# Kernel tuning notes

Hardware: AMD Instinct MI355X
Metric: run time of the kernel (lower is better)

## Reference

```python
import jax, jax.numpy as jnp
import numpy as np

DIM = 192
NUM_HEADS = 6
WINDOW = (2, 6, 12)
INPUT_RES = (8, 48, 180)
TYPE_OF_WINDOWS = (INPUT_RES[0] // WINDOW[0]) * (INPUT_RES[1] // WINDOW[1])  # 32
N_TOK = WINDOW[0] * WINDOW[1] * WINDOW[2]  # 144
NLON = INPUT_RES[2] // WINDOW[2]  # 15
TABLE_ROWS = WINDOW[0] ** 2 * WINDOW[1] ** 2 * (2 * WINDOW[2] - 1)  # 3312


def calculate_position_bias_indices(ws):
    wz, wh, ww = ws
    zi = np.arange(wz)
    zj = -np.arange(wz) * wz
    hi = np.arange(wh)
    hj = -np.arange(wh) * wh
    w = np.arange(ww)
    c1 = np.stack(np.meshgrid(zi, hi, w, indexing='ij')).reshape(3, -1)
    c2 = np.stack(np.meshgrid(zj, hj, w, indexing='ij')).reshape(3, -1)
    coords = (c1[:, :, None] - c2[:, None, :]).transpose(1, 2, 0).copy()
    coords[:, :, 2] += ww - 1
    coords[:, :, 1] *= 2 * ww - 1
    coords[:, :, 0] *= (2 * ww - 1) * wh * wh
    return coords.sum(-1)  # (N, N) in [0, TABLE_ROWS)


def setup_inputs() -> dict:
    key = jax.random.key(0)
    ks = jax.random.split(key, 7)
    B_ = NLON  # batch=1 times nLon window columns
    x = jax.random.normal(ks[0], (B_, TYPE_OF_WINDOWS, N_TOK, DIM), dtype=jnp.float32)
    mask = jax.random.normal(ks[1], (NLON, TYPE_OF_WINDOWS, N_TOK, N_TOK), dtype=jnp.float32)
    qkv_w = jax.random.normal(ks[2], (3 * DIM, DIM), dtype=jnp.float32) * 0.02
    qkv_b = jax.random.normal(ks[3], (3 * DIM,), dtype=jnp.float32) * 0.02
    proj_w = jax.random.normal(ks[4], (DIM, DIM), dtype=jnp.float32) * 0.02
    proj_b = jax.random.normal(ks[5], (DIM,), dtype=jnp.float32) * 0.02
    bias_table = jax.random.normal(ks[6], (TABLE_ROWS, TYPE_OF_WINDOWS, NUM_HEADS), dtype=jnp.float32) * 0.02
    position_index = jnp.asarray(calculate_position_bias_indices(WINDOW), dtype=jnp.int64)
    return {"x": x, "mask": mask, "qkv_w": qkv_w, "qkv_b": qkv_b,
            "proj_w": proj_w, "proj_b": proj_b, "bias_table": bias_table,
            "position_index": position_index}


def reference(x, mask, qkv_w, qkv_b, proj_w, proj_b, bias_table, position_index):
    B_, nW_, N, C = x.shape
    H = NUM_HEADS
    hd = C // H
    scale = hd ** (-0.5)
    # qkv projection: (B_, nW_, N, 3, H, hd)
    qkv = (jnp.einsum('bwnc,dc->bwnd', x, qkv_w) + qkv_b).reshape(B_, nW_, N, 3, H, hd)
    q = qkv[:, :, :, 0] * scale  # (B_, nW_, N, H, hd)
    k = qkv[:, :, :, 1]
    v = qkv[:, :, :, 2]
    # attention scores: (B_, H, nW_, N, N)
    attn = jnp.einsum('bwihd,bwjhd->bhwij', q, k)
    # gathered earth position bias -> (H, nW_, N, N)
    bias = bias_table[position_index.reshape(-1)]  # (N*N, nW_, H)
    bias = bias.reshape(N, N, nW_, H).transpose(3, 2, 0, 1)
    attn = attn + bias[None]
    # mask add: view (B_//nLon, nLon, H, nW_, N, N) + mask (nLon, 1, nW_, N, N)
    nLon = mask.shape[0]
    attn = attn.reshape(B_ // nLon, nLon, H, nW_, N, N) + mask[None, :, None]
    attn = attn.reshape(B_, H, nW_, N, N)
    attn = jax.nn.softmax(attn, axis=-1)
    out = jnp.einsum('bhwij,bwjhd->bwihd', attn, v).reshape(B_, nW_, N, C)
    out = jnp.einsum('bwnc,dc->bwnd', out, proj_w) + proj_b
    return out
```

## Files before the change

### kernel.cpp

```cpp
#include <hip/hip_runtime.h>
#include <hip/hip_bf16.h>

#define B_LON 15
#define NW    32
#define NTOK  144
#define DIM   192
#define NH    6
#define HD    32
#define K3    576
#define MROWS (B_LON*NW*NTOK)
#define NN    (NTOK*NTOK)
#define SCALE 0.17677669529663687f

typedef __attribute__((ext_vector_type(8))) short bf16x8;
typedef __attribute__((ext_vector_type(8))) unsigned short u16x8;
typedef __attribute__((ext_vector_type(4))) float f32x4;

__device__ inline unsigned short f2bf(float f) {
  __bf16 h = (__bf16)f;
  return __builtin_bit_cast(unsigned short, h);
}
__device__ inline float bf2f(unsigned short u) {
  union { unsigned int i; float f; } c;
  c.i = ((unsigned int)u) << 16;
  return c.f;
}

#define NX8 1658880
#define NQ8 13824
#define NP8 4608

__global__ __launch_bounds__(256) void conv_bf_k(
    const float* __restrict__ x, const float* __restrict__ qw,
    const float* __restrict__ pw,
    unsigned short* __restrict__ xbf, unsigned short* __restrict__ qwbf,
    unsigned short* __restrict__ pwbf) {
  const long gid = (long)blockIdx.x * 256 + threadIdx.x;
  const float* src;
  unsigned short* dst;
  long off;
  if (gid < NX8)            { src = x;  dst = xbf;  off = gid; }
  else if (gid < NX8 + NQ8) { src = qw; dst = qwbf; off = gid - NX8; }
  else                      { src = pw; dst = pwbf; off = gid - NX8 - NQ8; }
  const float4 a = ((const float4*)src)[off * 2];
  const float4 b = ((const float4*)src)[off * 2 + 1];
  u16x8 u = {f2bf(a.x), f2bf(a.y), f2bf(a.z), f2bf(a.w),
             f2bf(b.x), f2bf(b.y), f2bf(b.z), f2bf(b.w)};
  *(u16x8*)&dst[off * 8] = u;
}

__global__ __launch_bounds__(256) void bias_pre_k(
    const float* __restrict__ btab, const int* __restrict__ pos,
    unsigned short* __restrict__ biasb) {
  const int wh  = blockIdx.x;
  const int seg = blockIdx.y * 2304;
  unsigned short* dst = biasb + (size_t)wh * NN;
#pragma unroll
  for (int it = 0; it < 9; ++it) {
    const int e = seg + it * 256 + threadIdx.x;
    dst[e] = f2bf(btab[(size_t)pos[e] * (NW * NH) + wh]);
  }
}

__global__ __launch_bounds__(256) void qkv_gemm_k(
    const unsigned short* __restrict__ X, const unsigned short* __restrict__ W,
    const float* __restrict__ Bv,
    unsigned short* __restrict__ qb, unsigned short* __restrict__ kb,
    unsigned short* __restrict__ vb) {
  __shared__ unsigned short As[256 * 72];
  __shared__ unsigned short Bs[64 * 72];
  const int t    = threadIdx.x;
  const int n0   = blockIdx.x * 64;
  const int m0   = blockIdx.y * 256;
  const int w    = t >> 6;
  const int lane = t & 63;
  const int ln15 = lane & 15;
  const int quad = lane >> 4;
  const int srow = t >> 3;
  const int schk = (t & 7) * 8;

  f32x4 acc[4][4];
#pragma unroll
  for (int i = 0; i < 4; ++i)
#pragma unroll
    for (int j = 0; j < 4; ++j) acc[i][j] = (f32x4){0.f, 0.f, 0.f, 0.f};

  for (int k0 = 0; k0 < 192; k0 += 64) {
    u16x8 ar[8], br[2];
#pragma unroll
    for (int rr = 0; rr < 8; ++rr)
      ar[rr] = *(const u16x8*)&X[(size_t)(m0 + rr * 32 + srow) * 192 + k0 + schk];
#pragma unroll
    for (int rr = 0; rr < 2; ++rr)
      br[rr] = *(const u16x8*)&W[(size_t)(n0 + rr * 32 + srow) * 192 + k0 + schk];
    __syncthreads();
#pragma unroll
    for (int rr = 0; rr < 8; ++rr)
      *(u16x8*)&As[(rr * 32 + srow) * 72 + schk] = ar[rr];
#pragma unroll
    for (int rr = 0; rr < 2; ++rr)
      *(u16x8*)&Bs[(rr * 32 + srow) * 72 + schk] = br[rr];
    __syncthreads();

#pragma unroll
    for (int half = 0; half < 2; ++half) {
      bf16x8 af[4], bf[4];
#pragma unroll
      for (int mt = 0; mt < 4; ++mt)
        af[mt] = *(bf16x8*)&As[(w * 64 + mt * 16 + ln15) * 72 + half * 32 + quad * 8];
#pragma unroll
      for (int nt = 0; nt < 4; ++nt)
        bf[nt] = *(bf16x8*)&Bs[(nt * 16 + ln15) * 72 + half * 32 + quad * 8];
#pragma unroll
      for (int mt = 0; mt < 4; ++mt)
#pragma unroll
        for (int nt = 0; nt < 4; ++nt)
          acc[mt][nt] = __builtin_amdgcn_mfma_f32_16x16x32_bf16(
              af[mt], bf[nt], acc[mt][nt], 0, 0, 0);
    }
    __syncthreads();
  }

  const int s   = n0 / 192;
  const int nr  = n0 % 192;
  const float sc2 = (s == 0) ? SCALE : 1.0f;
  unsigned short* dst = (s == 0) ? qb : (s == 1 ? kb : vb);
#pragma unroll
  for (int nt = 0; nt < 4; ++nt) {
    const int colg = n0 + nt * 16 + ln15;
    const int h    = (nr + nt * 16 + ln15) >> 5;
    const int dd   = (nr + nt * 16 + ln15) & 31;
    const float bias = Bv[colg];
#pragma unroll
    for (int mt = 0; mt < 4; ++mt) {
#pragma unroll
      for (int r = 0; r < 4; ++r) {
        const int m  = m0 + w * 64 + mt * 16 + quad * 4 + r;
        const int bw = m / NTOK;
        const int n  = m % NTOK;
        const unsigned short val = f2bf((acc[mt][nt][r] + bias) * sc2);
        if (s < 2)
          dst[((size_t)(bw * NH + h) * NTOK + n) * HD + dd] = val;
        else
          dst[((size_t)(bw * NH + h) * HD + dd) * NTOK + n] = val;
      }
    }
  }
}

__global__ __launch_bounds__(192, 3) void attn_k(
    const unsigned short* __restrict__ qbuf, const unsigned short* __restrict__ kbuf,
    const unsigned short* __restrict__ vbuf, const float* __restrict__ mask,
    const unsigned short* __restrict__ biasb, unsigned short* __restrict__ ao) {
  __shared__ unsigned short Ks[NTOK * 36];
  __shared__ unsigned short Vs[32 * 160];
  __shared__ unsigned short Ps[3 * 16 * 168];

  const int t    = threadIdx.x;
  const int wave = t / 64;
  const int lane = t & 63;
  const int ln15 = lane & 15;
  const int quad = lane >> 4;
  const int idx  = blockIdx.x;
  const int h    = idx / 480;
  const int bw   = idx % 480;
  const int w    = bw & 31;
  const int wh   = w * NH + h;
  const size_t hb = (size_t)(bw * NH + h) * (NTOK * HD);
  const unsigned short* qh = qbuf + hb;
  const float* maskp = mask + (size_t)bw * NN;
  const unsigned short* biasp = biasb + (size_t)wh * NN;
  unsigned short* ps = &Ps[wave * 16 * 168];

  for (int it = t; it < 576; it += 192) {
    const int row = it >> 2;
    const int col = (it & 3) * 8;
    *(u16x8*)&Ks[row * 36 + col] = *(const u16x8*)&kbuf[hb + row * HD + col];
  }
  for (int it = t; it < 576; it += 192) {
    const int row = it / 18;
    const int col = (it % 18) * 8;
    *(u16x8*)&Vs[row * 160 + col] = *(const u16x8*)&vbuf[hb + row * NTOK + col];
  }
  if (t < 64) {
    u16x8 z = {0, 0, 0, 0, 0, 0, 0, 0};
    *(u16x8*)&Vs[(t >> 1) * 160 + 144 + (t & 1) * 8] = z;
  }
  {
    ushort4 z = {0, 0, 0, 0};
    *(ushort4*)&ps[(lane >> 2) * 168 + 144 + (lane & 3) * 4] = z;
  }
  __syncthreads();

  for (int g = wave * 3; g < wave * 3 + 3; ++g) {
    const int i0 = g * 16;
    const int ib = i0 + quad * 4;

    const bf16x8 qf = *(const bf16x8*)&qh[(i0 + ln15) * HD + quad * 8];
    f32x4 s[9];
#pragma unroll
    for (int jt = 0; jt < 9; ++jt) {
      const bf16x8 kf = *(const bf16x8*)&Ks[(jt * 16 + ln15) * 36 + quad * 8];
      s[jt] = (f32x4){0.f, 0.f, 0.f, 0.f};
      s[jt] = __builtin_amdgcn_mfma_f32_16x16x32_bf16(qf, kf, s[jt], 0, 0, 0);
    }

#pragma unroll
    for (int jt = 0; jt < 9; ++jt) {
      const int j = jt * 16 + ln15;
#pragma unroll
      for (int r = 0; r < 4; ++r) {
        const int ij = (ib + r) * NTOK + j;
        s[jt][r] += bf2f(biasp[ij]) + maskp[ij];
      }
    }

    float rinv[4];
#pragma unroll
    for (int r = 0; r < 4; ++r) {
      float mx = s[0][r];
#pragma unroll
      for (int jt = 1; jt < 9; ++jt) mx = fmaxf(mx, s[jt][r]);
#pragma unroll
      for (int off = 1; off < 16; off <<= 1) mx = fmaxf(mx, __shfl_xor(mx, off));
      float sum = 0.f;
#pragma unroll
      for (int jt = 0; jt < 9; ++jt) {
        const float e = __expf(s[jt][r] - mx);
        s[jt][r] = e;
        sum += e;
      }
#pragma unroll
      for (int off = 1; off < 16; off <<= 1) sum += __shfl_xor(sum, off);
      rinv[r] = 1.0f / sum;
    }

#pragma unroll
    for (int jt = 0; jt < 9; ++jt)
#pragma unroll
      for (int r = 0; r < 4; ++r)
        ps[(quad * 4 + r) * 168 + jt * 16 + ln15] = f2bf(s[jt][r]);

    f32x4 o[2] = {{0.f, 0.f, 0.f, 0.f}, {0.f, 0.f, 0.f, 0.f}};
#pragma unroll
    for (int kt = 0; kt < 5; ++kt) {
      const bf16x8 pf = *(const bf16x8*)&ps[ln15 * 168 + kt * 32 + quad * 8];
#pragma unroll
      for (int nt = 0; nt < 2; ++nt) {
        const bf16x8 vf = *(const bf16x8*)&Vs[(nt * 16 + ln15) * 160 + kt * 32 + quad * 8];
        o[nt] = __builtin_amdgcn_mfma_f32_16x16x32_bf16(pf, vf, o[nt], 0, 0, 0);
      }
    }

#pragma unroll
    for (int nt = 0; nt < 2; ++nt)
#pragma unroll
      for (int r = 0; r < 4; ++r)
        ao[(size_t)(bw * NTOK + ib + r) * DIM + h * HD + nt * 16 + ln15] =
            f2bf(o[nt][r] * rinv[r]);
  }
}

__global__ __launch_bounds__(256) void proj_gemm_k(
    const unsigned short* __restrict__ AO, const unsigned short* __restrict__ W,
    const float* __restrict__ Bv, float* __restrict__ out) {
  __shared__ unsigned short As[256 * 72];
  __shared__ unsigned short Bs[64 * 72];
  const int t    = threadIdx.x;
  const int n0   = blockIdx.x * 64;
  const int m0   = blockIdx.y * 256;
  const int w    = t >> 6;
  const int lane = t & 63;
  const int ln15 = lane & 15;
  const int quad = lane >> 4;
  const int srow = t >> 3;
  const int schk = (t & 7) * 8;

  f32x4 acc[4][4];
#pragma unroll
  for (int i = 0; i < 4; ++i)
#pragma unroll
    for (int j = 0; j < 4; ++j) acc[i][j] = (f32x4){0.f, 0.f, 0.f, 0.f};

  for (int k0 = 0; k0 < 192; k0 += 64) {
    u16x8 ar[8], br[2];
#pragma unroll
    for (int rr = 0; rr < 8; ++rr)
      ar[rr] = *(const u16x8*)&AO[(size_t)(m0 + rr * 32 + srow) * 192 + k0 + schk];
#pragma unroll
    for (int rr = 0; rr < 2; ++rr)
      br[rr] = *(const u16x8*)&W[(size_t)(n0 + rr * 32 + srow) * 192 + k0 + schk];
    __syncthreads();
#pragma unroll
    for (int rr = 0; rr < 8; ++rr)
      *(u16x8*)&As[(rr * 32 + srow) * 72 + schk] = ar[rr];
#pragma unroll
    for (int rr = 0; rr < 2; ++rr)
      *(u16x8*)&Bs[(rr * 32 + srow) * 72 + schk] = br[rr];
    __syncthreads();

#pragma unroll
    for (int half = 0; half < 2; ++half) {
      bf16x8 af[4], bf[4];
#pragma unroll
      for (int mt = 0; mt < 4; ++mt)
        af[mt] = *(bf16x8*)&As[(w * 64 + mt * 16 + ln15) * 72 + half * 32 + quad * 8];
#pragma unroll
      for (int nt = 0; nt < 4; ++nt)
        bf[nt] = *(bf16x8*)&Bs[(nt * 16 + ln15) * 72 + half * 32 + quad * 8];
#pragma unroll
      for (int mt = 0; mt < 4; ++mt)
#pragma unroll
        for (int nt = 0; nt < 4; ++nt)
          acc[mt][nt] = __builtin_amdgcn_mfma_f32_16x16x32_bf16(
              af[mt], bf[nt], acc[mt][nt], 0, 0, 0);
    }
    __syncthreads();
  }

#pragma unroll
  for (int nt = 0; nt < 4; ++nt) {
    const int colg = n0 + nt * 16 + ln15;
    const float bias = Bv[colg];
#pragma unroll
    for (int mt = 0; mt < 4; ++mt) {
#pragma unroll
      for (int r = 0; r < 4; ++r) {
        const int m = m0 + w * 64 + mt * 16 + quad * 4 + r;
        out[(size_t)m * 192 + colg] = acc[mt][nt][r] + bias;
      }
    }
  }
}

extern "C" void kernel_launch(void* const* d_in, const int* in_sizes, int n_in,
                              void* d_out, int out_size, void* d_ws, size_t ws_size,
                              hipStream_t stream) {
  const float* x      = (const float*)d_in[0];
  const float* mask   = (const float*)d_in[1];
  const float* qkv_w  = (const float*)d_in[2];
  const float* qkv_b  = (const float*)d_in[3];
  const float* proj_w = (const float*)d_in[4];
  const float* proj_b = (const float*)d_in[5];
  const float* btab   = (const float*)d_in[6];
  const int*   pos    = (const int*)d_in[7];
  float* out = (float*)d_out;

  unsigned short* ws = (unsigned short*)d_ws;
  const size_t sz = (size_t)MROWS * DIM;
  unsigned short* qbuf  = ws;
  unsigned short* kbuf  = ws + sz;
  unsigned short* vbuf  = ws + 2 * sz;
  unsigned short* aobuf = ws + 3 * sz + 256;
  unsigned short* biasb = ws + 4 * sz + 1024;
  unsigned short* xbf   = biasb + (size_t)192 * NN;
  unsigned short* qwbf  = xbf + sz;
  unsigned short* pwbf  = qwbf + (size_t)K3 * DIM;

  conv_bf_k<<<NX8 / 256 + NQ8 / 256 + NP8 / 256, 256, 0, stream>>>(
      x, qkv_w, proj_w, xbf, qwbf, pwbf);
  bias_pre_k<<<dim3(NW * NH, 9), 256, 0, stream>>>(btab, pos, biasb);
  qkv_gemm_k<<<dim3(K3 / 64, MROWS / 256), 256, 0, stream>>>(
      xbf, qwbf, qkv_b, qbuf, kbuf, vbuf);
  attn_k<<<NH * 480, 192, 0, stream>>>(
      qbuf, kbuf, vbuf, mask, biasb, aobuf);
  proj_gemm_k<<<dim3(DIM / 64, MROWS / 256), 256, 0, stream>>>(
      aobuf, pwbf, proj_b, out);
}
```

Before: 300.9 us.

## Fuse x bf16 conversion into QKV GEMM and keep full-K row tiles resident

The separate fp32-to-bf16 pass over x is removed. The QKV GEMM now loads fp32 x rows directly, converts them, and holds a full 128x192 bf16 tile in shared memory, then loops over all 576 output columns. Both GEMMs read weights directly from global memory (cache-resident) instead of staging them in LDS. This avoids one full write and one full read of x in bf16 and cuts redundant A-tile loads across N blocks. In exchange, weight fragments are fetched from global/L2 inside the MFMA loop, and each block does more serial work with a smaller M tile.

```diff
diff --git a/kernel.cpp b/kernel.cpp
--- a/kernel.cpp
+++ b/kernel.cpp
@@ -26,22 +26,18 @@
   return c.f;
 }
 
-#define NX8 1658880
 #define NQ8 13824
 #define NP8 4608
 
 __global__ __launch_bounds__(256) void conv_bf_k(
-    const float* __restrict__ x, const float* __restrict__ qw,
-    const float* __restrict__ pw,
-    unsigned short* __restrict__ xbf, unsigned short* __restrict__ qwbf,
-    unsigned short* __restrict__ pwbf) {
+    const float* __restrict__ qw, const float* __restrict__ pw,
+    unsigned short* __restrict__ qwbf, unsigned short* __restrict__ pwbf) {
   const long gid = (long)blockIdx.x * 256 + threadIdx.x;
   const float* src;
   unsigned short* dst;
   long off;
-  if (gid < NX8)            { src = x;  dst = xbf;  off = gid; }
-  else if (gid < NX8 + NQ8) { src = qw; dst = qwbf; off = gid - NX8; }
-  else                      { src = pw; dst = pwbf; off = gid - NX8 - NQ8; }
+  if (gid < NQ8) { src = qw; dst = qwbf; off = gid; }
+  else           { src = pw; dst = pwbf; off = gid - NQ8; }
   const float4 a = ((const float4*)src)[off * 2];
   const float4 b = ((const float4*)src)[off * 2 + 1];
   u16x8 u = {f2bf(a.x), f2bf(a.y), f2bf(a.z), f2bf(a.w),
@@ -63,86 +59,77 @@
 }
 
 __global__ __launch_bounds__(256) void qkv_gemm_k(
-    const unsigned short* __restrict__ X, const unsigned short* __restrict__ W,
+    const float* __restrict__ X, const unsigned short* __restrict__ W,
     const float* __restrict__ Bv,
     unsigned short* __restrict__ qb, unsigned short* __restrict__ kb,
     unsigned short* __restrict__ vb) {
-  __shared__ unsigned short As[256 * 72];
-  __shared__ unsigned short Bs[64 * 72];
+  __shared__ unsigned short As[128 * 200];
   const int t    = threadIdx.x;
-  const int n0   = blockIdx.x * 64;
-  const int m0   = blockIdx.y * 256;
+  const int m0   = blockIdx.x * 128;
   const int w    = t >> 6;
   const int lane = t & 63;
   const int ln15 = lane & 15;
   const int quad = lane >> 4;
-  const int srow = t >> 3;
-  const int schk = (t & 7) * 8;
-
-  f32x4 acc[4][4];
-#pragma unroll
-  for (int i = 0; i < 4; ++i)
-#pragma unroll
-    for (int j = 0; j < 4; ++j) acc[i][j] = (f32x4){0.f, 0.f, 0.f, 0.f};
-
-  for (int k0 = 0; k0 < 192; k0 += 64) {
-    u16x8 ar[8], br[2];
-#pragma unroll
-    for (int rr = 0; rr < 8; ++rr)
-      ar[rr] = *(const u16x8*)&X[(size_t)(m0 + rr * 32 + srow) * 192 + k0 + schk];
-#pragma unroll
-    for (int rr = 0; rr < 2; ++rr)
-      br[rr] = *(const u16x8*)&W[(size_t)(n0 + rr * 32 + srow) * 192 + k0 + schk];
-    __syncthreads();
-#pragma unroll
-    for (int rr = 0; rr < 8; ++rr)
-      *(u16x8*)&As[(rr * 32 + srow) * 72 + schk] = ar[rr];
-#pragma unroll
-    for (int rr = 0; rr < 2; ++rr)
-      *(u16x8*)&Bs[(rr * 32 + srow) * 72 + schk] = br[rr];
-    __syncthreads();
-
-#pragma unroll
-    for (int half = 0; half < 2; ++half) {
-      bf16x8 af[4], bf[4];
-#pragma unroll
-      for (int mt = 0; mt < 4; ++mt)
-        af[mt] = *(bf16x8*)&As[(w * 64 + mt * 16 + ln15) * 72 + half * 32 + quad * 8];
-#pragma unroll
-      for (int nt = 0; nt < 4; ++nt)
-        bf[nt] = *(bf16x8*)&Bs[(nt * 16 + ln15) * 72 + half * 32 + quad * 8];
-#pragma unroll
-      for (int mt = 0; mt < 4; ++mt)
+
+  for (int it = t; it < 128 * 48; it += 256) {
+    const int row = it / 48;
+    const int c4  = it % 48;
+    const float4 a = *(const float4*)&X[(size_t)(m0 + row) * 192 + c4 * 4];
+    ushort4 u = {f2bf(a.x), f2bf(a.y), f2bf(a.z), f2bf(a.w)};
+    *(ushort4*)&As[row * 200 + c4 * 4] = u;
+  }
+  __syncthreads();
+
+  for (int s = 0; s < 3; ++s) {
+    const float sc2 = (s == 0) ? SCALE : 1.0f;
+    unsigned short* dst = (s == 0) ? qb : (s == 1 ? kb : vb);
+    for (int nc = 0; nc < 3; ++nc) {
+      const int n0 = s * 192 + nc * 64;
+      const int nr = nc * 64;
+
+      f32x4 acc[2][4];
+#pragma unroll
+      for (int i = 0; i < 2; ++i)
+#pragma unroll
+        for (int j = 0; j < 4; ++j) acc[i][j] = (f32x4){0.f, 0.f, 0.f, 0.f};
+
+#pragma unroll
+      for (int k0 = 0; k0 < 192; k0 += 32) {
+        bf16x8 af[2], bfr[4];
+#pragma unroll
+        for (int mt = 0; mt < 2; ++mt)
+          af[mt] = *(bf16x8*)&As[(w * 32 + mt * 16 + ln15) * 200 + k0 + quad * 8];
 #pragma unroll
         for (int nt = 0; nt < 4; ++nt)
-          acc[mt][nt] = __builtin_amdgcn_mfma_f32_16x16x32_bf16(
-              af[mt], bf[nt], acc[mt][nt], 0, 0, 0);
-    }
-    __syncthreads();
-  }
-
-  const int s   = n0 / 192;
-  const int nr  = n0 % 192;
-  const float sc2 = (s == 0) ? SCALE : 1.0f;
-  unsigned short* dst = (s == 0) ? qb : (s == 1 ? kb : vb);
-#pragma unroll
-  for (int nt = 0; nt < 4; ++nt) {
-    const int colg = n0 + nt * 16 + ln15;
-    const int h    = (nr + nt * 16 + ln15) >> 5;
-    const int dd   = (nr + nt * 16 + ln15) & 31;
-    const float bias = Bv[colg];
-#pragma unroll
-    for (int mt = 0; mt < 4; ++mt) {
-#pragma unroll
-      for (int r = 0; r < 4; ++r) {
-        const int m  = m0 + w * 64 + mt * 16 + quad * 4 + r;
-        const int bw = m / NTOK;
-        const int n  = m % NTOK;
-        const unsigned short val = f2bf((acc[mt][nt][r] + bias) * sc2);
-        if (s < 2)
-          dst[((size_t)(bw * NH + h) * NTOK + n) * HD + dd] = val;
-        else
-          dst[((size_t)(bw * NH + h) * HD + dd) * NTOK + n] = val;
+          bfr[nt] = *(const bf16x8*)&W[(size_t)(n0 + nt * 16 + ln15) * 192 + k0 + quad * 8];
+#pragma unroll
+        for (int mt = 0; mt < 2; ++mt)
+#pragma unroll
+          for (int nt = 0; nt < 4; ++nt)
+            acc[mt][nt] = __builtin_amdgcn_mfma_f32_16x16x32_bf16(
+                af[mt], bfr[nt], acc[mt][nt], 0, 0, 0);
+      }
+
+#pragma unroll
+      for (int nt = 0; nt < 4; ++nt) {
+        const int colg = n0 + nt * 16 + ln15;
+        const int h    = (nr + nt * 16 + ln15) >> 5;
+        const int dd   = (nr + nt * 16 + ln15) & 31;
+        const float bias = Bv[colg];
+#pragma unroll
+        for (int mt = 0; mt < 2; ++mt) {
+#pragma unroll
+          for (int r = 0; r < 4; ++r) {
+            const int m  = m0 + w * 32 + mt * 16 + quad * 4 + r;
+            const int bw = m / NTOK;
+            const int n  = m % NTOK;
+            const unsigned short val = f2bf((acc[mt][nt][r] + bias) * sc2);
+            if (s < 2)
+              dst[((size_t)(bw * NH + h) * NTOK + n) * HD + dd] = val;
+            else
+              dst[((size_t)(bw * NH + h) * HD + dd) * NTOK + n] = val;
+          }
+        }
       }
     }
   }
@@ -264,70 +251,59 @@
 __global__ __launch_bounds__(256) void proj_gemm_k(
     const unsigned short* __restrict__ AO, const unsigned short* __restrict__ W,
     const float* __restrict__ Bv, float* __restrict__ out) {
-  __shared__ unsigned short As[256 * 72];
-  __shared__ unsigned short Bs[64 * 72];
+  __shared__ unsigned short As[128 * 200];
   const int t    = threadIdx.x;
-  const int n0   = blockIdx.x * 64;
-  const int m0   = blockIdx.y * 256;
+  const int m0   = blockIdx.x * 128;
   const int w    = t >> 6;
   const int lane = t & 63;
   const int ln15 = lane & 15;
   const int quad = lane >> 4;
-  const int srow = t >> 3;
-  const int schk = (t & 7) * 8;
-
-  f32x4 acc[4][4];
-#pragma unroll
-  for (int i = 0; i < 4; ++i)
-#pragma unroll
-    for (int j = 0; j < 4; ++j) acc[i][j] = (f32x4){0.f, 0.f, 0.f, 0.f};
-
-  for (int k0 = 0; k0 < 192; k0 += 64) {
-    u16x8 ar[8], br[2];
-#pragma unroll
-    for (int rr = 0; rr < 8; ++rr)
-      ar[rr] = *(const u16x8*)&AO[(size_t)(m0 + rr * 32 + srow) * 192 + k0 + schk];
-#pragma unroll
-    for (int rr = 0; rr < 2; ++rr)
-      br[rr] = *(const u16x8*)&W[(size_t)(n0 + rr * 32 + srow) * 192 + k0 + schk];
-    __syncthreads();
-#pragma unroll
-    for (int rr = 0; rr < 8; ++rr)
-      *(u16x8*)&As[(rr * 32 + srow) * 72 + schk] = ar[rr];
-#pragma unroll
-    for (int rr = 0; rr < 2; ++rr)
-      *(u16x8*)&Bs[(rr * 32 + srow) * 72 + schk] = br[rr];
-    __syncthreads();
-
-#pragma unroll
-    for (int half = 0; half < 2; ++half) {
-      bf16x8 af[4], bf[4];
-#pragma unroll
-      for (int mt = 0; mt < 4; ++mt)
-        af[mt] = *(bf16x8*)&As[(w * 64 + mt * 16 + ln15) * 72 + half * 32 + quad * 8];
+
+  for (int it = t; it < 128 * 24; it += 256) {
+    const int row = it / 24;
+    const int c8  = it % 24;
+    *(u16x8*)&As[row * 200 + c8 * 8] =
+        *(const u16x8*)&AO[(size_t)(m0 + row) * 192 + c8 * 8];
+  }
+  __syncthreads();
+
+  for (int nc = 0; nc < 3; ++nc) {
+    const int n0 = nc * 64;
+
+    f32x4 acc[2][4];
+#pragma unroll
+    for (int i = 0; i < 2; ++i)
+#pragma unroll
+      for (int j = 0; j < 4; ++j) acc[i][j] = (f32x4){0.f, 0.f, 0.f, 0.f};
+
+#pragma unroll
+    for (int k0 = 0; k0 < 192; k0 += 32) {
+      bf16x8 af[2], bfr[4];
+#pragma unroll
+      for (int mt = 0; mt < 2; ++mt)
+        af[mt] = *(bf16x8*)&As[(w * 32 + mt * 16 + ln15) * 200 + k0 + quad * 8];
 #pragma unroll
       for (int nt = 0; nt < 4; ++nt)
-        bf[nt] = *(bf16x8*)&Bs[(nt * 16 + ln15) * 72 + half * 32 + quad * 8];
-#pragma unroll
-      for (int mt = 0; mt < 4; ++mt)
+        bfr[nt] = *(const bf16x8*)&W[(size_t)(n0 + nt * 16 + ln15) * 192 + k0 + quad * 8];
+#pragma unroll
+      for (int mt = 0; mt < 2; ++mt)
 #pragma unroll
         for (int nt = 0; nt < 4; ++nt)
           acc[mt][nt] = __builtin_amdgcn_mfma_f32_16x16x32_bf16(
-              af[mt], bf[nt], acc[mt][nt], 0, 0, 0);
-    }
-    __syncthreads();
-  }
-
-#pragma unroll
-  for (int nt = 0; nt < 4; ++nt) {
-    const int colg = n0 + nt * 16 + ln15;
-    const float bias = Bv[colg];
-#pragma unroll
-    for (int mt = 0; mt < 4; ++mt) {
-#pragma unroll
-      for (int r = 0; r < 4; ++r) {
-        const int m = m0 + w * 64 + mt * 16 + quad * 4 + r;
-        out[(size_t)m * 192 + colg] = acc[mt][nt][r] + bias;
+              af[mt], bfr[nt], acc[mt][nt], 0, 0, 0);
+    }
+
+#pragma unroll
+    for (int nt = 0; nt < 4; ++nt) {
+      const int colg = n0 + nt * 16 + ln15;
+      const float bias = Bv[colg];
+#pragma unroll
+      for (int mt = 0; mt < 2; ++mt) {
+#pragma unroll
+        for (int r = 0; r < 4; ++r) {
+          const int m = m0 + w * 32 + mt * 16 + quad * 4 + r;
+          out[(size_t)m * 192 + colg] = acc[mt][nt][r] + bias;
+        }
       }
     }
   }
@@ -353,17 +329,15 @@
   unsigned short* vbuf  = ws + 2 * sz;
   unsigned short* aobuf = ws + 3 * sz + 256;
   unsigned short* biasb = ws + 4 * sz + 1024;
-  unsigned short* xbf   = biasb + (size_t)192 * NN;
-  unsigned short* qwbf  = xbf + sz;
+  unsigned short* qwbf  = biasb + (size_t)192 * NN;
   unsigned short* pwbf  = qwbf + (size_t)K3 * DIM;
 
-  conv_bf_k<<<NX8 / 256 + NQ8 / 256 + NP8 / 256, 256, 0, stream>>>(
-      x, qkv_w, proj_w, xbf, qwbf, pwbf);
+  conv_bf_k<<<(NQ8 + NP8) / 256, 256, 0, stream>>>(qkv_w, proj_w, qwbf, pwbf);
   bias_pre_k<<<dim3(NW * NH, 9), 256, 0, stream>>>(btab, pos, biasb);
-  qkv_gemm_k<<<dim3(K3 / 64, MROWS / 256), 256, 0, stream>>>(
-      xbf, qwbf, qkv_b, qbuf, kbuf, vbuf);
+  qkv_gemm_k<<<MROWS / 128, 256, 0, stream>>>(
+      x, qwbf, qkv_b, qbuf, kbuf, vbuf);
   attn_k<<<NH * 480, 192, 0, stream>>>(
       qbuf, kbuf, vbuf, mask, biasb, aobuf);
-  proj_gemm_k<<<dim3(DIM / 64, MROWS / 256), 256, 0, stream>>>(
+  proj_gemm_k<<<MROWS / 128, 256, 0, stream>>>(
       aobuf, pwbf, proj_b, out);
 }
```

After: 371.3 us. 1.23x slower.
